# Optimization experiments

Measured on AMD Instinct MI355X. Metric: run time of the kernel, lower is better.

Reference implementation:

```python
import jax, jax.numpy as jnp
import numpy as np


def setup_inputs() -> dict:
    key = jax.random.key(0)
    k1, k2, k3, k4 = jax.random.split(key, 4)
    dim, b, q_len, c_len = 1024, 16, 1024, 2048
    q = jax.random.normal(k1, (q_len, b, dim), dtype=jnp.float32)
    c = jax.random.normal(k2, (c_len, b, dim), dtype=jnp.float32)
    # torch nn.Linear weights: [out_features, in_features]
    W_in = jax.random.normal(k3, (dim, dim), dtype=jnp.float32) * (dim ** -0.5)
    W_out = jax.random.normal(k4, (dim, 2 * dim), dtype=jnp.float32) * ((2 * dim) ** -0.5)
    return {"q": q, "c": c, "W_in": W_in, "W_out": W_out}


def reference(q, c, W_in, W_out):
    # q: [q_len, b, dim] -> [b, q_len, dim]; c: [c_len, b, dim] -> [b, c_len, dim]
    qb = jnp.transpose(q, (1, 0, 2))
    cb = jnp.transpose(c, (1, 0, 2))
    qb = jnp.einsum('bqd,ed->bqe', qb, W_in)            # linear_in (no bias)
    score = jnp.einsum('bqd,bkd->bqk', qb, cb)          # unscaled QK^T
    score = jax.nn.softmax(score, axis=-1)              # [b, q_len, c_len]
    ctx = jnp.einsum('bqk,bkd->bqd', score, cb)         # score @ c
    cat = jnp.concatenate([ctx, qb], axis=-1)           # [b, q_len, 2*dim]
    out = jnp.tanh(jnp.einsum('bqf,df->bqd', cat, W_out))
    return (jnp.transpose(out, (1, 0, 2)), score)       # ([q_len,b,dim], [b,q_len,c_len])
```

## Files before the change

### kernel.cpp

```cpp
#include <hip/hip_runtime.h>
#include <hip/hip_bf16.h>
#include <stdint.h>


typedef __bf16 bf16x8 __attribute__((ext_vector_type(8)));
typedef float floatx16 __attribute__((ext_vector_type(16)));

__device__ __forceinline__ unsigned short f2bf_rne(float f) {
  unsigned int u = __float_as_uint(f);
  u += 0x7FFFu + ((u >> 16) & 1u);
  return (unsigned short)(u >> 16);
}
__device__ __forceinline__ float bf2f(unsigned short h) {
  return __uint_as_float(((unsigned int)h) << 16);
}

__device__ __forceinline__ void async_load16(const void* g, void* l) {
  __builtin_amdgcn_global_load_lds(
      (const __attribute__((address_space(1))) void*)g,
      (__attribute__((address_space(3))) void*)l,
      16, 0, 0);
}

__device__ __forceinline__ int kperm(int r) {
  return ((r >> 1) ^ (r >> 3)) & 3;
}
__device__ __forceinline__ int frag_slot(int r, int kb) {
  return (r * 4 + (kb ^ kperm(r))) * 8;
}

__global__ __launch_bounds__(256) void split_kernel(
    const float* __restrict__ x, unsigned short* __restrict__ hi,
    unsigned short* __restrict__ lo, long n4)
{
  long i = (long)blockIdx.x * 256 + threadIdx.x;
  if (i >= n4) return;
  float4 v = ((const float4*)x)[i];
  ushort4 h;
  h.x = f2bf_rne(v.x); h.y = f2bf_rne(v.y);
  h.z = f2bf_rne(v.z); h.w = f2bf_rne(v.w);
  ((ushort4*)hi)[i] = h;
  if (lo) {
    ushort4 l;
    l.x = f2bf_rne(v.x - bf2f(h.x));
    l.y = f2bf_rne(v.y - bf2f(h.y));
    l.z = f2bf_rne(v.z - bf2f(h.z));
    l.w = f2bf_rne(v.w - bf2f(h.w));
    ((ushort4*)lo)[i] = l;
  }
}

__global__ __launch_bounds__(256) void transpose_kernel(
    const float* __restrict__ c, unsigned short* __restrict__ ct)
{
  __shared__ unsigned short t[64 * 68];
  int k0 = blockIdx.x * 64;
  int d0 = blockIdx.y * 64;
  int b  = blockIdx.z;
  int tid = threadIdx.x;
  #pragma unroll
  for (int p4 = 0; p4 < 4; ++p4) {
    int idx = p4 * 256 + tid;
    int kr = idx >> 4;
    int dc = (idx & 15) * 4;
    float4 v = *(const float4*)&c[(long)(k0 + kr) * 16384 + (long)b * 1024 + d0 + dc];
    ushort4 h;
    h.x = f2bf_rne(v.x); h.y = f2bf_rne(v.y);
    h.z = f2bf_rne(v.z); h.w = f2bf_rne(v.w);
    *(ushort4*)&t[kr * 68 + dc] = h;
  }
  __syncthreads();
  #pragma unroll
  for (int p4 = 0; p4 < 4; ++p4) {
    int idx = p4 * 256 + tid;
    int dr = idx >> 4;
    int kc = (idx & 15) * 4;
    ushort4 o;
    o.x = t[(kc + 0) * 68 + dr];
    o.y = t[(kc + 1) * 68 + dr];
    o.z = t[(kc + 2) * 68 + dr];
    o.w = t[(kc + 3) * 68 + dr];
    *(ushort4*)&ct[(long)b * 2097152 + (long)(d0 + dr) * 2048 + k0 + kc] = o;
  }
}

__global__ __launch_bounds__(256) void softmax_kernel(
    float* __restrict__ S, unsigned short* __restrict__ P)
{
  __shared__ float sred[8];
  long row = blockIdx.x;
  float* p = S + row * 2048;
  int tid = threadIdx.x;
  int lane = tid & 63, w = tid >> 6;
  float4 v0 = ((float4*)p)[tid];
  float4 v1 = ((float4*)p)[tid + 256];
  float m = fmaxf(fmaxf(fmaxf(v0.x, v0.y), fmaxf(v0.z, v0.w)),
                  fmaxf(fmaxf(v1.x, v1.y), fmaxf(v1.z, v1.w)));
  #pragma unroll
  for (int off = 32; off; off >>= 1) m = fmaxf(m, __shfl_xor(m, off));
  if (lane == 0) sred[w] = m;
  __syncthreads();
  m = fmaxf(fmaxf(sred[0], sred[1]), fmaxf(sred[2], sred[3]));
  v0.x = __expf(v0.x - m); v0.y = __expf(v0.y - m);
  v0.z = __expf(v0.z - m); v0.w = __expf(v0.w - m);
  v1.x = __expf(v1.x - m); v1.y = __expf(v1.y - m);
  v1.z = __expf(v1.z - m); v1.w = __expf(v1.w - m);
  float s = v0.x + v0.y + v0.z + v0.w + v1.x + v1.y + v1.z + v1.w;
  #pragma unroll
  for (int off = 32; off; off >>= 1) s += __shfl_xor(s, off);
  if (lane == 0) sred[4 + w] = s;
  __syncthreads();
  s = sred[4] + sred[5] + sred[6] + sred[7];
  float inv = 1.0f / s;
  v0.x *= inv; v0.y *= inv; v0.z *= inv; v0.w *= inv;
  v1.x *= inv; v1.y *= inv; v1.z *= inv; v1.w *= inv;
  ((float4*)p)[tid] = v0;
  ((float4*)p)[tid + 256] = v1;
  unsigned short* pp = P + row * 2048;
  ushort4 b0, b1;
  b0.x = f2bf_rne(v0.x); b0.y = f2bf_rne(v0.y);
  b0.z = f2bf_rne(v0.z); b0.w = f2bf_rne(v0.w);
  b1.x = f2bf_rne(v1.x); b1.y = f2bf_rne(v1.y);
  b1.z = f2bf_rne(v1.z); b1.w = f2bf_rne(v1.w);
  ((ushort4*)pp)[tid] = b0;
  ((ushort4*)pp)[tid + 256] = b1;
}

template<int SPLIT, int MODE>
__global__ __launch_bounds__(512, 2) void gemm_kernel(
    const unsigned short* __restrict__ Ah, const unsigned short* __restrict__ Al,
    long sAb, long ldA,
    const unsigned short* __restrict__ Bh, const unsigned short* __restrict__ Bl,
    long sBb, long ldB,
    void* __restrict__ Cp, long sCb, long ldC,
    unsigned short* __restrict__ P1, unsigned short* __restrict__ P2,
    int K, int SM, int SN, int GM)
{
  __shared__ __align__(16) unsigned short lds[65536];

  const int tid  = threadIdx.x;
  const int lane = tid & 63;
  const int w    = tid >> 6;
  const int wm   = w >> 2;
  const int wn   = w & 3;
  const int bz   = blockIdx.z;

  const int flat = blockIdx.x + gridDim.x * blockIdx.y;
  const int sub  = flat & 7;
  const int g    = flat >> 3;
  const long mt  = (long)(sub % GM) * SM + (g / SN);
  const long nt  = (long)(sub / GM) * SN + (g % SN);
  const long m0  = mt * 256;
  const long n0  = nt * 256;

  const unsigned short* a0 = Ah + bz * sAb + m0 * ldA;
  const unsigned short* a1 = SPLIT ? (Al + bz * sAb + m0 * ldA) : a0;
  const unsigned short* b0 = Bh + bz * sBb + n0 * ldB;
  const unsigned short* b1 = SPLIT ? (Bl + bz * sBb + n0 * ldB) : b0;

  const int s0r = tid >> 2,        s1r = (512 + tid) >> 2;
  const int s0k = (tid & 3) ^ kperm(s0r);
  const int s1k = ((512 + tid) & 3) ^ kperm(s1r);
  const long offA0 = (long)s0r * ldA + s0k * 8;
  const long offA1 = (long)s1r * ldA + s1k * 8;
  const long offB0 = (long)s0r * ldB + s0k * 8;
  const long offB1 = (long)s1r * ldB + s1k * 8;
  const int d0 = w * 512;
  const int d1 = 4096 + w * 512;

  floatx16 acc[4][2] = {};

  const int rA = wm * 128 + (lane & 31);
  const int rB = wn * 64 + (lane & 31);
  const int kbase = lane >> 5;

  if constexpr (SPLIT) {
    const int nk = K / 32;

    auto stageE = [&](int k, int h) {
      const int slot = (2 * k + h) & 3;
      const unsigned short* As = h ? a1 : a0;
      const unsigned short* Bs = h ? b1 : b0;
      const long ks = (long)k * 32;
      const int ab = slot * 8192;
      const int bb = 32768 + slot * 8192;
      async_load16(As + offA0 + ks, &lds[ab + d0]);
      async_load16(As + offA1 + ks, &lds[ab + d1]);
      async_load16(Bs + offB0 + ks, &lds[bb + d0]);
      async_load16(Bs + offB1 + ks, &lds[bb + d1]);
    };

    stageE(0, 0); stageE(0, 1);

    for (int k = 0; k < nk; ++k) {
      asm volatile("s_waitcnt vmcnt(4)" ::: "memory");
      __builtin_amdgcn_s_barrier();
      __builtin_amdgcn_sched_barrier(0);

      if (k + 1 < nk) { stageE(k + 1, 0); stageE(k + 1, 1); }
      __builtin_amdgcn_sched_barrier(0);

      const unsigned short* Ah_t = &lds[((2 * k) & 3) * 8192];
      const unsigned short* Bh_t = &lds[32768 + ((2 * k) & 3) * 8192];
      const unsigned short* Al_t = &lds[((2 * k + 1) & 3) * 8192];
      const unsigned short* Bl_t = &lds[32768 + ((2 * k + 1) & 3) * 8192];

      bf16x8 fah[2][4], fbh[2][2];
      __builtin_amdgcn_s_setprio(1);
      #pragma unroll
      for (int kk = 0; kk < 2; ++kk) {
        const int kb = kbase + kk * 2;
        #pragma unroll
        for (int j = 0; j < 2; ++j)
          fbh[kk][j] = *(const bf16x8*)&Bh_t[frag_slot(rB + j * 32, kb)];
        #pragma unroll
        for (int i = 0; i < 4; ++i)
          fah[kk][i] = *(const bf16x8*)&Ah_t[frag_slot(rA + i * 32, kb)];
        #pragma unroll
        for (int i = 0; i < 4; ++i) {
          acc[i][0] = __builtin_amdgcn_mfma_f32_32x32x16_bf16(fah[kk][i], fbh[kk][0], acc[i][0], 0, 0, 0);
          acc[i][1] = __builtin_amdgcn_mfma_f32_32x32x16_bf16(fah[kk][i], fbh[kk][1], acc[i][1], 0, 0, 0);
        }
      }
      __builtin_amdgcn_s_setprio(0);

      if (k + 1 < nk) asm volatile("s_waitcnt vmcnt(8)" ::: "memory");
      else            asm volatile("s_waitcnt vmcnt(0)" ::: "memory");
      __builtin_amdgcn_s_barrier();
      __builtin_amdgcn_sched_barrier(0);

      __builtin_amdgcn_s_setprio(1);
      #pragma unroll
      for (int kk = 0; kk < 2; ++kk) {
        const int kb = kbase + kk * 2;
        bf16x8 fbl[2], fal[4];
        #pragma unroll
        for (int j = 0; j < 2; ++j)
          fbl[j] = *(const bf16x8*)&Bl_t[frag_slot(rB + j * 32, kb)];
        #pragma unroll
        for (int i = 0; i < 4; ++i)
          fal[i] = *(const bf16x8*)&Al_t[frag_slot(rA + i * 32, kb)];
        #pragma unroll
        for (int i = 0; i < 4; ++i) {
          acc[i][0] = __builtin_amdgcn_mfma_f32_32x32x16_bf16(fah[kk][i], fbl[0], acc[i][0], 0, 0, 0);
          acc[i][1] = __builtin_amdgcn_mfma_f32_32x32x16_bf16(fah[kk][i], fbl[1], acc[i][1], 0, 0, 0);
        }
        #pragma unroll
        for (int i = 0; i < 4; ++i) {
          acc[i][0] = __builtin_amdgcn_mfma_f32_32x32x16_bf16(fal[i], fbh[kk][0], acc[i][0], 0, 0, 0);
          acc[i][1] = __builtin_amdgcn_mfma_f32_32x32x16_bf16(fal[i], fbh[kk][1], acc[i][1], 0, 0, 0);
        }
      }
      __builtin_amdgcn_s_setprio(0);
    }
  } else {
    const int nkt = K / 32;

    auto stage = [&](int vt2) {
      const int slot = vt2 & 3;
      const long ks = (long)vt2 * 32;
      const int ab = slot * 8192;
      const int bb = 32768 + slot * 8192;
      async_load16(a0 + offA0 + ks, &lds[ab + d0]);
      async_load16(a0 + offA1 + ks, &lds[ab + d1]);
      async_load16(b0 + offB0 + ks, &lds[bb + d0]);
      async_load16(b0 + offB1 + ks, &lds[bb + d1]);
    };

    stage(0); stage(1); stage(2);

    for (int vt = 0; vt < nkt; ++vt) {
      const int ahead = nkt - 1 - vt;
      if (ahead >= 2)      asm volatile("s_waitcnt vmcnt(8)" ::: "memory");
      else if (ahead == 1) asm volatile("s_waitcnt vmcnt(4)" ::: "memory");
      else                 asm volatile("s_waitcnt vmcnt(0)" ::: "memory");
      __builtin_amdgcn_s_barrier();
      __builtin_amdgcn_sched_barrier(0);

      if (vt + 3 < nkt) stage(vt + 3);
      __builtin_amdgcn_sched_barrier(0);

      const unsigned short* At = &lds[(vt & 3) * 8192];
      const unsigned short* Bt = &lds[32768 + (vt & 3) * 8192];

      __builtin_amdgcn_s_setprio(1);
      #pragma unroll
      for (int kk = 0; kk < 2; ++kk) {
        const int kb = kbase + kk * 2;
        bf16x8 fb[2], fa[4];
        #pragma unroll
        for (int j = 0; j < 2; ++j)
          fb[j] = *(const bf16x8*)&Bt[frag_slot(rB + j * 32, kb)];
        #pragma unroll
        for (int i = 0; i < 4; ++i)
          fa[i] = *(const bf16x8*)&At[frag_slot(rA + i * 32, kb)];
        #pragma unroll
        for (int i = 0; i < 4; ++i) {
          acc[i][0] = __builtin_amdgcn_mfma_f32_32x32x16_bf16(fa[i], fb[0], acc[i][0], 0, 0, 0);
          acc[i][1] = __builtin_amdgcn_mfma_f32_32x32x16_bf16(fa[i], fb[1], acc[i][1], 0, 0, 0);
        }
      }
      __builtin_amdgcn_s_setprio(0);
    }
  }

  #pragma unroll
  for (int i = 0; i < 4; ++i) {
    #pragma unroll
    for (int j = 0; j < 2; ++j) {
      #pragma unroll
      for (int t = 0; t < 16; ++t) {
        long rg = m0 + wm * 128 + i * 32 + (t & 3) + 8 * (t >> 2) + 4 * (lane >> 5);
        long cg = n0 + wn * 64 + j * 32 + (lane & 31);
        float v = acc[i][j][t];
        if (MODE == 0) {
          ((float*)Cp)[bz * sCb + rg * ldC + cg] = v;
        } else if (MODE == 1) {
          ((unsigned short*)Cp)[bz * sCb + rg * ldC + cg] = f2bf_rne(v);
        } else if (MODE == 2) {
          long qq = rg & 1023, bb = rg >> 10;
          ((float*)Cp)[(qq * 16 + bb) * 1024 + cg] = tanhf(v);
        } else {
          unsigned short hv = f2bf_rne(v);
          unsigned short lv = f2bf_rne(v - bf2f(hv));
          P1[rg * 1024 + cg] = hv;
          P2[rg * 1024 + cg] = lv;
          long bb = rg & 15, qq = rg >> 4;
          ((unsigned short*)Cp)[(bb * 1024 + qq) * 2048 + 1024 + cg] = hv;
        }
      }
    }
  }
}

extern "C" void kernel_launch(void* const* d_in, const int* in_sizes, int n_in,
                              void* d_out, int out_size, void* d_ws, size_t ws_size,
                              hipStream_t stream)
{
  const float* q    = (const float*)d_in[0];
  const float* c    = (const float*)d_in[1];
  const float* Win  = (const float*)d_in[2];
  const float* Wout = (const float*)d_in[3];

  char* ws = (char*)d_ws;
  const size_t MB = 1024u * 1024u;

  unsigned short* qh  = (unsigned short*)(ws);
  unsigned short* ch  = (unsigned short*)(ws);
  unsigned short* pb  = (unsigned short*)(ws);
  unsigned short* qbh = (unsigned short*)(ws + 64 * MB);
  unsigned short* qbl = (unsigned short*)(ws + 96 * MB);
  unsigned short* ct  = (unsigned short*)(ws + 64 * MB);
  unsigned short* cat = (unsigned short*)(ws + 128 * MB);
  unsigned short* Wh  = (unsigned short*)(ws + 192 * MB);
  unsigned short* Wl  = (unsigned short*)(ws + 194 * MB);
  unsigned short* Wo  = (unsigned short*)(ws + 196 * MB);

  unsigned short* ql  = (unsigned short*)d_out;
  unsigned short* cl  = (unsigned short*)d_out;
  float* out0  = (float*)d_out;
  float* score = (float*)d_out + 16777216;

  split_kernel<<<16384, 256, 0, stream>>>(q,    qh, ql,      4194304L);
  split_kernel<<<1024,  256, 0, stream>>>(Win,  Wh, Wl,      262144L);
  split_kernel<<<2048,  256, 0, stream>>>(Wout, Wo, nullptr, 524288L);

  gemm_kernel<1, 3><<<dim3(32, 8, 1), 512, 0, stream>>>(
      qh, ql, 0L, 1024L, Wh, Wl, 0L, 1024L,
      (void*)cat, 0L, 0L, qbh, qbl, 1024, 8, 4, 8);

  split_kernel<<<32768, 256, 0, stream>>>(c, ch, cl, 8388608L);

  gemm_kernel<1, 0><<<dim3(4, 8, 16), 512, 0, stream>>>(
      qbh, qbl, 1024L, 16384L, ch, cl, 1024L, 16384L,
      (void*)score, 2097152L, 2048L, nullptr, nullptr, 1024, 2, 2, 2);

  transpose_kernel<<<dim3(32, 16, 16), 256, 0, stream>>>(c, ct);
  softmax_kernel<<<16384, 256, 0, stream>>>(score, pb);

  gemm_kernel<0, 1><<<dim3(4, 4, 16), 512, 0, stream>>>(
      pb, nullptr, 2097152L, 2048L, ct, nullptr, 2097152L, 2048L,
      (void*)cat, 2097152L, 2048L, nullptr, nullptr, 2048, 1, 2, 4);

  gemm_kernel<0, 2><<<dim3(32, 8, 1), 512, 0, stream>>>(
      cat, nullptr, 0L, 2048L, Wo, nullptr, 0L, 2048L,
      (void*)out0, 0L, 0L, nullptr, nullptr, 2048, 8, 4, 8);

  (void)in_sizes; (void)n_in; (void)out_size; (void)ws_size;
}
```

Baseline: 903.0 us.

## Split GEMM main loop into barrier-separated LDS-read and MFMA phases

Restructures both the split (hi/lo bf16) and plain GEMM main loops into alternating phases. In each phase all waves first read LDS fragments and issue async global loads, then run MFMAs, with a workgroup barrier between phases. Prefetch issue is spread across phases (hi and lo halves staged at different points) and the waitcnt points move to the end of each K step. The goal is to keep waves in lockstep so LDS reads and MFMA bursts from different waves do not contend, in the style of a ping-pong schedule. The cost is several extra s_barriers per K step, which can add stalls if the phases are unbalanced.

```diff
diff --git a/kernel.cpp b/kernel.cpp
--- a/kernel.cpp
+++ b/kernel.cpp
@@ -28,6 +28,9 @@
 __device__ __forceinline__ int frag_slot(int r, int kb) {
   return (r * 4 + (kb ^ kperm(r))) * 8;
 }
+
+#define SBAR0() __builtin_amdgcn_sched_barrier(0)
+#define PHASE_BAR() do { SBAR0(); __builtin_amdgcn_s_barrier(); SBAR0(); } while (0)
 
 __global__ __launch_bounds__(256) void split_kernel(
     const float* __restrict__ x, unsigned short* __restrict__ hi,
@@ -191,67 +194,105 @@
     };
 
     stageE(0, 0); stageE(0, 1);
+    if (nk > 1) stageE(1, 0);
+    if (nk > 1) asm volatile("s_waitcnt vmcnt(8)" ::: "memory");
+    else        asm volatile("s_waitcnt vmcnt(4)" ::: "memory");
+    PHASE_BAR();
 
     for (int k = 0; k < nk; ++k) {
-      asm volatile("s_waitcnt vmcnt(4)" ::: "memory");
-      __builtin_amdgcn_s_barrier();
-      __builtin_amdgcn_sched_barrier(0);
-
-      if (k + 1 < nk) { stageE(k + 1, 0); stageE(k + 1, 1); }
-      __builtin_amdgcn_sched_barrier(0);
-
       const unsigned short* Ah_t = &lds[((2 * k) & 3) * 8192];
       const unsigned short* Bh_t = &lds[32768 + ((2 * k) & 3) * 8192];
       const unsigned short* Al_t = &lds[((2 * k + 1) & 3) * 8192];
       const unsigned short* Bl_t = &lds[32768 + ((2 * k + 1) & 3) * 8192];
 
       bf16x8 fah[2][4], fbh[2][2];
+
+      #pragma unroll
+      for (int j = 0; j < 2; ++j)
+        fbh[0][j] = *(const bf16x8*)&Bh_t[frag_slot(rB + j * 32, kbase)];
+      #pragma unroll
+      for (int i = 0; i < 4; ++i)
+        fah[0][i] = *(const bf16x8*)&Ah_t[frag_slot(rA + i * 32, kbase)];
+      if (k + 1 < nk) stageE(k + 1, 1);
+      PHASE_BAR();
       __builtin_amdgcn_s_setprio(1);
       #pragma unroll
-      for (int kk = 0; kk < 2; ++kk) {
-        const int kb = kbase + kk * 2;
-        #pragma unroll
-        for (int j = 0; j < 2; ++j)
-          fbh[kk][j] = *(const bf16x8*)&Bh_t[frag_slot(rB + j * 32, kb)];
-        #pragma unroll
-        for (int i = 0; i < 4; ++i)
-          fah[kk][i] = *(const bf16x8*)&Ah_t[frag_slot(rA + i * 32, kb)];
-        #pragma unroll
-        for (int i = 0; i < 4; ++i) {
-          acc[i][0] = __builtin_amdgcn_mfma_f32_32x32x16_bf16(fah[kk][i], fbh[kk][0], acc[i][0], 0, 0, 0);
-          acc[i][1] = __builtin_amdgcn_mfma_f32_32x32x16_bf16(fah[kk][i], fbh[kk][1], acc[i][1], 0, 0, 0);
-        }
+      for (int i = 0; i < 4; ++i) {
+        acc[i][0] = __builtin_amdgcn_mfma_f32_32x32x16_bf16(fah[0][i], fbh[0][0], acc[i][0], 0, 0, 0);
+        acc[i][1] = __builtin_amdgcn_mfma_f32_32x32x16_bf16(fah[0][i], fbh[0][1], acc[i][1], 0, 0, 0);
       }
       __builtin_amdgcn_s_setprio(0);
-
+      PHASE_BAR();
+
+      #pragma unroll
+      for (int j = 0; j < 2; ++j)
+        fbh[1][j] = *(const bf16x8*)&Bh_t[frag_slot(rB + j * 32, kbase + 2)];
+      #pragma unroll
+      for (int i = 0; i < 4; ++i)
+        fah[1][i] = *(const bf16x8*)&Ah_t[frag_slot(rA + i * 32, kbase + 2)];
+      PHASE_BAR();
+      __builtin_amdgcn_s_setprio(1);
+      #pragma unroll
+      for (int i = 0; i < 4; ++i) {
+        acc[i][0] = __builtin_amdgcn_mfma_f32_32x32x16_bf16(fah[1][i], fbh[1][0], acc[i][0], 0, 0, 0);
+        acc[i][1] = __builtin_amdgcn_mfma_f32_32x32x16_bf16(fah[1][i], fbh[1][1], acc[i][1], 0, 0, 0);
+      }
+      __builtin_amdgcn_s_setprio(0);
       if (k + 1 < nk) asm volatile("s_waitcnt vmcnt(8)" ::: "memory");
       else            asm volatile("s_waitcnt vmcnt(0)" ::: "memory");
-      __builtin_amdgcn_s_barrier();
-      __builtin_amdgcn_sched_barrier(0);
-
-      __builtin_amdgcn_s_setprio(1);
-      #pragma unroll
-      for (int kk = 0; kk < 2; ++kk) {
-        const int kb = kbase + kk * 2;
+      PHASE_BAR();
+
+      {
         bf16x8 fbl[2], fal[4];
         #pragma unroll
         for (int j = 0; j < 2; ++j)
-          fbl[j] = *(const bf16x8*)&Bl_t[frag_slot(rB + j * 32, kb)];
+          fbl[j] = *(const bf16x8*)&Bl_t[frag_slot(rB + j * 32, kbase)];
         #pragma unroll
         for (int i = 0; i < 4; ++i)
-          fal[i] = *(const bf16x8*)&Al_t[frag_slot(rA + i * 32, kb)];
-        #pragma unroll
-        for (int i = 0; i < 4; ++i) {
-          acc[i][0] = __builtin_amdgcn_mfma_f32_32x32x16_bf16(fah[kk][i], fbl[0], acc[i][0], 0, 0, 0);
-          acc[i][1] = __builtin_amdgcn_mfma_f32_32x32x16_bf16(fah[kk][i], fbl[1], acc[i][1], 0, 0, 0);
-        }
-        #pragma unroll
-        for (int i = 0; i < 4; ++i) {
-          acc[i][0] = __builtin_amdgcn_mfma_f32_32x32x16_bf16(fal[i], fbh[kk][0], acc[i][0], 0, 0, 0);
-          acc[i][1] = __builtin_amdgcn_mfma_f32_32x32x16_bf16(fal[i], fbh[kk][1], acc[i][1], 0, 0, 0);
-        }
-      }
-      __builtin_amdgcn_s_setprio(0);
+          fal[i] = *(const bf16x8*)&Al_t[frag_slot(rA + i * 32, kbase)];
+        if (k + 2 < nk) stageE(k + 2, 0);
+        PHASE_BAR();
+        __builtin_amdgcn_s_setprio(1);
+        #pragma unroll
+        for (int i = 0; i < 4; ++i) {
+          acc[i][0] = __builtin_amdgcn_mfma_f32_32x32x16_bf16(fah[0][i], fbl[0], acc[i][0], 0, 0, 0);
+          acc[i][1] = __builtin_amdgcn_mfma_f32_32x32x16_bf16(fah[0][i], fbl[1], acc[i][1], 0, 0, 0);
+        }
+        #pragma unroll
+        for (int i = 0; i < 4; ++i) {
+          acc[i][0] = __builtin_amdgcn_mfma_f32_32x32x16_bf16(fal[i], fbh[0][0], acc[i][0], 0, 0, 0);
+          acc[i][1] = __builtin_amdgcn_mfma_f32_32x32x16_bf16(fal[i], fbh[0][1], acc[i][1], 0, 0, 0);
+        }
+        __builtin_amdgcn_s_setprio(0);
+        PHASE_BAR();
+      }
+
+      {
+        bf16x8 fbl[2], fal[4];
+        #pragma unroll
+        for (int j = 0; j < 2; ++j)
+          fbl[j] = *(const bf16x8*)&Bl_t[frag_slot(rB + j * 32, kbase + 2)];
+        #pragma unroll
+        for (int i = 0; i < 4; ++i)
+          fal[i] = *(const bf16x8*)&Al_t[frag_slot(rA + i * 32, kbase + 2)];
+        PHASE_BAR();
+        __builtin_amdgcn_s_setprio(1);
+        #pragma unroll
+        for (int i = 0; i < 4; ++i) {
+          acc[i][0] = __builtin_amdgcn_mfma_f32_32x32x16_bf16(fah[1][i], fbl[0], acc[i][0], 0, 0, 0);
+          acc[i][1] = __builtin_amdgcn_mfma_f32_32x32x16_bf16(fah[1][i], fbl[1], acc[i][1], 0, 0, 0);
+        }
+        #pragma unroll
+        for (int i = 0; i < 4; ++i) {
+          acc[i][0] = __builtin_amdgcn_mfma_f32_32x32x16_bf16(fal[i], fbh[1][0], acc[i][0], 0, 0, 0);
+          acc[i][1] = __builtin_amdgcn_mfma_f32_32x32x16_bf16(fal[i], fbh[1][1], acc[i][1], 0, 0, 0);
+        }
+        __builtin_amdgcn_s_setprio(0);
+        if (k + 2 < nk)      asm volatile("s_waitcnt vmcnt(8)" ::: "memory");
+        else if (k + 1 < nk) asm volatile("s_waitcnt vmcnt(4)" ::: "memory");
+        else                 asm volatile("s_waitcnt vmcnt(0)" ::: "memory");
+        PHASE_BAR();
+      }
     }
   } else {
     const int nkt = K / 32;
@@ -268,39 +309,55 @@
     };
 
     stage(0); stage(1); stage(2);
+    asm volatile("s_waitcnt vmcnt(8)" ::: "memory");
+    PHASE_BAR();
 
     for (int vt = 0; vt < nkt; ++vt) {
       const int ahead = nkt - 1 - vt;
-      if (ahead >= 2)      asm volatile("s_waitcnt vmcnt(8)" ::: "memory");
-      else if (ahead == 1) asm volatile("s_waitcnt vmcnt(4)" ::: "memory");
-      else                 asm volatile("s_waitcnt vmcnt(0)" ::: "memory");
-      __builtin_amdgcn_s_barrier();
-      __builtin_amdgcn_sched_barrier(0);
-
-      if (vt + 3 < nkt) stage(vt + 3);
-      __builtin_amdgcn_sched_barrier(0);
-
       const unsigned short* At = &lds[(vt & 3) * 8192];
       const unsigned short* Bt = &lds[32768 + (vt & 3) * 8192];
 
-      __builtin_amdgcn_s_setprio(1);
-      #pragma unroll
-      for (int kk = 0; kk < 2; ++kk) {
-        const int kb = kbase + kk * 2;
+      {
         bf16x8 fb[2], fa[4];
         #pragma unroll
         for (int j = 0; j < 2; ++j)
-          fb[j] = *(const bf16x8*)&Bt[frag_slot(rB + j * 32, kb)];
+          fb[j] = *(const bf16x8*)&Bt[frag_slot(rB + j * 32, kbase)];
         #pragma unroll
         for (int i = 0; i < 4; ++i)
-          fa[i] = *(const bf16x8*)&At[frag_slot(rA + i * 32, kb)];
+          fa[i] = *(const bf16x8*)&At[frag_slot(rA + i * 32, kbase)];
+        if (vt + 3 < nkt) stage(vt + 3);
+        PHASE_BAR();
+        __builtin_amdgcn_s_setprio(1);
         #pragma unroll
         for (int i = 0; i < 4; ++i) {
           acc[i][0] = __builtin_amdgcn_mfma_f32_32x32x16_bf16(fa[i], fb[0], acc[i][0], 0, 0, 0);
           acc[i][1] = __builtin_amdgcn_mfma_f32_32x32x16_bf16(fa[i], fb[1], acc[i][1], 0, 0, 0);
         }
-      }
-      __builtin_amdgcn_s_setprio(0);
+        __builtin_amdgcn_s_setprio(0);
+        PHASE_BAR();
+      }
+
+      {
+        bf16x8 fb[2], fa[4];
+        #pragma unroll
+        for (int j = 0; j < 2; ++j)
+          fb[j] = *(const bf16x8*)&Bt[frag_slot(rB + j * 32, kbase + 2)];
+        #pragma unroll
+        for (int i = 0; i < 4; ++i)
+          fa[i] = *(const bf16x8*)&At[frag_slot(rA + i * 32, kbase + 2)];
+        PHASE_BAR();
+        __builtin_amdgcn_s_setprio(1);
+        #pragma unroll
+        for (int i = 0; i < 4; ++i) {
+          acc[i][0] = __builtin_amdgcn_mfma_f32_32x32x16_bf16(fa[i], fb[0], acc[i][0], 0, 0, 0);
+          acc[i][1] = __builtin_amdgcn_mfma_f32_32x32x16_bf16(fa[i], fb[1], acc[i][1], 0, 0, 0);
+        }
+        __builtin_amdgcn_s_setprio(0);
+        if (ahead >= 3)      asm volatile("s_waitcnt vmcnt(8)" ::: "memory");
+        else if (ahead == 2) asm volatile("s_waitcnt vmcnt(4)" ::: "memory");
+        else if (ahead == 1) asm volatile("s_waitcnt vmcnt(0)" ::: "memory");
+        PHASE_BAR();
+      }
     }
   }
 
```

Result: no change. 916.9 us (+1.5%).
